# Kernel optimization log

Hardware: AMD Instinct MI355X
Metric: run time of the kernel (lower is better)

The kernel has to match this reference:

```python
import jax, jax.numpy as jnp
import numpy as np

TAU = 1.0  # initial_temperature, non-trainable
EPS = 1e-10


def setup_inputs() -> dict:
    key = jax.random.key(0)
    ks = jax.random.split(key, 5)
    B, D, E, A = 8192, 1024, 32, 128
    x = jax.random.normal(ks[0], (B, D), dtype=jnp.float32)
    W_att = jax.random.normal(ks[1], (E, D), dtype=jnp.float32) * (1.0 / np.sqrt(D))
    b_att = jnp.zeros((E,), dtype=jnp.float32)
    adaptive_bias = jnp.zeros((E,), dtype=jnp.float32)
    W_strat = jax.random.normal(ks[2], (E, A, D), dtype=jnp.float32) * (1.0 / np.sqrt(D))
    b_strat = jnp.zeros((E, A), dtype=jnp.float32)
    gumbel_u = jax.random.uniform(ks[3], (B, E), dtype=jnp.float32)
    return {"x": x, "W_att": W_att, "b_att": b_att, "adaptive_bias": adaptive_bias,
            "W_strat": W_strat, "b_strat": b_strat, "gumbel_u": gumbel_u}


def reference(x, W_att, b_att, adaptive_bias, W_strat, b_strat, gumbel_u):
    # Gating: linear + adaptive bias, then gumbel-softmax with temperature TAU
    logits = x @ W_att.T + b_att + adaptive_bias            # [B, E]
    g = -jnp.log(-jnp.log(gumbel_u + EPS) + EPS)            # gumbel noise [B, E]
    weights = jax.nn.softmax((logits + g) / TAU, axis=-1)   # [B, E] soft selection
    # Per-strategy outputs: each strategy is Linear(D -> A)
    strat_out = jnp.einsum('bd,ead->bea', x, W_strat) + b_strat  # [B, E, A]
    # Weighted combine (superposition)
    out = jnp.einsum('be,bea->ba', weights, strat_out)      # [B, A]
    return out
```

## Files before the change

### kernel.cpp

```cpp
#include <hip/hip_runtime.h>
#include <stdint.h>

typedef unsigned short u16;
typedef __attribute__((ext_vector_type(4))) float f32x4;
typedef __attribute__((ext_vector_type(8))) short short8;
typedef __attribute__((ext_vector_type(8))) unsigned short u16x8;

static constexpr int Bq = 8192;
static constexpr int Dq = 1024;
static constexpr int Eq = 32;
static constexpr int Aq = 128;
static constexpr int NSTRAT = 4096;

__device__ inline u16 f32_to_bf16_rne(float f) {
    uint32_t u = __float_as_uint(f);
    uint32_t r = 0x7fffu + ((u >> 16) & 1u);
    return (u16)((u + r) >> 16);
}
__device__ inline float bf16_to_f32(u16 h) {
    return __uint_as_float(((uint32_t)h) << 16);
}
__device__ inline void gload_lds16(const u16* g, u16* l) {
    __builtin_amdgcn_global_load_lds(
        (const __attribute__((address_space(1))) void*)g,
        (__attribute__((address_space(3))) void*)l, 16, 0, 0);
}

__global__ __launch_bounds__(256) void cvt_fused(const float* __restrict__ x,
                                                 const float* __restrict__ Ws,
                                                 u16* __restrict__ xb) {
    size_t i = ((size_t)blockIdx.x * 256 + threadIdx.x) * 8;
    const size_t XN = (size_t)Bq * Dq;
    const float* src;
    if (i < XN) {
        src = x + i;
    } else {
        size_t j = i - XN;
        int rp = (int)(j >> 10);
        int e = rp & 31;
        int a = rp >> 5;
        src = Ws + ((size_t)((e << 7) + a) << 10) + (j & 1023);
    }
    f32x4 a4 = *(const f32x4*)(src);
    f32x4 b4 = *(const f32x4*)(src + 4);
    u16x8 o;
    o[0] = f32_to_bf16_rne(a4[0]); o[1] = f32_to_bf16_rne(a4[1]);
    o[2] = f32_to_bf16_rne(a4[2]); o[3] = f32_to_bf16_rne(a4[3]);
    o[4] = f32_to_bf16_rne(b4[0]); o[5] = f32_to_bf16_rne(b4[1]);
    o[6] = f32_to_bf16_rne(b4[2]); o[7] = f32_to_bf16_rne(b4[3]);
    *(u16x8*)(xb + i) = o;
}

#define FBAR do { asm volatile("" ::: "memory"); __builtin_amdgcn_s_barrier(); asm volatile("" ::: "memory"); } while (0)
#define LGKM0 asm volatile("s_waitcnt lgkmcnt(0)" ::: "memory")
#define VMCNT(n) asm volatile("s_waitcnt vmcnt(" #n ")" ::: "memory")
#define SB __builtin_amdgcn_sched_barrier(0)
#define PRIO1 __builtin_amdgcn_s_setprio(1)
#define PRIO0 __builtin_amdgcn_s_setprio(0)
#define MF(a, b, c) __builtin_amdgcn_mfma_f32_16x16x32_bf16(a, b, c, 0, 0, 0)


#define STAGE_A(buf, h, kt) do { \
    gload_lds16(agA + (size_t)((h)*128) * 1024 + (size_t)(kt) * 64, (u16*)&lds[buf][h][tid * 8]); \
    gload_lds16(agA + (size_t)((h)*128 + 64) * 1024 + (size_t)(kt) * 64, (u16*)&lds[buf][h][4096 + tid * 8]); \
} while (0)
#define STAGE_B(buf, h, kt) do { \
    gload_lds16(agB + (size_t)((h)*128) * 1024 + (size_t)(kt) * 64, (u16*)&lds[buf][2 + (h)][tid * 8]); \
    gload_lds16(agB + (size_t)((h)*128 + 64) * 1024 + (size_t)(kt) * 64, (u16*)&lds[buf][2 + (h)][4096 + tid * 8]); \
} while (0)

#define LDA8(DST, ABASE, mq) do { \
    DST[0] = *(const short8*)((ABASE) + (mq)*4096 + 0*1024 + aoff0); \
    DST[1] = *(const short8*)((ABASE) + (mq)*4096 + 0*1024 + aoff1); \
    DST[2] = *(const short8*)((ABASE) + (mq)*4096 + 1*1024 + aoff0); \
    DST[3] = *(const short8*)((ABASE) + (mq)*4096 + 1*1024 + aoff1); \
    DST[4] = *(const short8*)((ABASE) + (mq)*4096 + 2*1024 + aoff0); \
    DST[5] = *(const short8*)((ABASE) + (mq)*4096 + 2*1024 + aoff1); \
    DST[6] = *(const short8*)((ABASE) + (mq)*4096 + 3*1024 + aoff0); \
    DST[7] = *(const short8*)((ABASE) + (mq)*4096 + 3*1024 + aoff1); \
} while (0)
#define LDB4(DST, BBASE, nq) do { \
    DST[0] = *(const short8*)((BBASE) + (nq)*2048 + 0*1024 + boff0); \
    DST[1] = *(const short8*)((BBASE) + (nq)*2048 + 0*1024 + boff1); \
    DST[2] = *(const short8*)((BBASE) + (nq)*2048 + 1*1024 + boff0); \
    DST[3] = *(const short8*)((BBASE) + (nq)*2048 + 1*1024 + boff1); \
} while (0)

#define QUAD(mq, nq, AS, BS) do { \
    acc[(mq)*4+0][(nq)*2+0] = MF(AS[0], BS[0], acc[(mq)*4+0][(nq)*2+0]); \
    acc[(mq)*4+0][(nq)*2+1] = MF(AS[0], BS[2], acc[(mq)*4+0][(nq)*2+1]); \
    acc[(mq)*4+1][(nq)*2+0] = MF(AS[2], BS[0], acc[(mq)*4+1][(nq)*2+0]); \
    acc[(mq)*4+1][(nq)*2+1] = MF(AS[2], BS[2], acc[(mq)*4+1][(nq)*2+1]); \
    acc[(mq)*4+2][(nq)*2+0] = MF(AS[4], BS[0], acc[(mq)*4+2][(nq)*2+0]); \
    acc[(mq)*4+2][(nq)*2+1] = MF(AS[4], BS[2], acc[(mq)*4+2][(nq)*2+1]); \
    acc[(mq)*4+3][(nq)*2+0] = MF(AS[6], BS[0], acc[(mq)*4+3][(nq)*2+0]); \
    acc[(mq)*4+3][(nq)*2+1] = MF(AS[6], BS[2], acc[(mq)*4+3][(nq)*2+1]); \
    acc[(mq)*4+0][(nq)*2+0] = MF(AS[1], BS[1], acc[(mq)*4+0][(nq)*2+0]); \
    acc[(mq)*4+0][(nq)*2+1] = MF(AS[1], BS[3], acc[(mq)*4+0][(nq)*2+1]); \
    acc[(mq)*4+1][(nq)*2+0] = MF(AS[3], BS[1], acc[(mq)*4+1][(nq)*2+0]); \
    acc[(mq)*4+1][(nq)*2+1] = MF(AS[3], BS[3], acc[(mq)*4+1][(nq)*2+1]); \
    acc[(mq)*4+2][(nq)*2+0] = MF(AS[5], BS[1], acc[(mq)*4+2][(nq)*2+0]); \
    acc[(mq)*4+2][(nq)*2+1] = MF(AS[5], BS[3], acc[(mq)*4+2][(nq)*2+1]); \
    acc[(mq)*4+3][(nq)*2+0] = MF(AS[7], BS[1], acc[(mq)*4+3][(nq)*2+0]); \
    acc[(mq)*4+3][(nq)*2+1] = MF(AS[7], BS[3], acc[(mq)*4+3][(nq)*2+1]); \
} while (0)

#define GITER(t, TAIL) do { \
     \
    LDB4(Bs0, Bbase0, 0); \
    STAGE_A(1, 0, (t) + 1); \
    SB; FBAR; LGKM0; SB; \
    PRIO1; QUAD(0, 0, As0, Bs0); PRIO0; SB; FBAR; \
     \
    LDB4(Bs1, Bbase0, 1); \
    STAGE_A(1, 1, (t) + 1); \
    SB; FBAR; LGKM0; SB; \
    PRIO1; QUAD(0, 1, As0, Bs1); PRIO0; SB; FBAR; \
     \
    LDA8(As1, Abase0, 1); \
    if (!(TAIL)) STAGE_B(0, 0, (t) + 2); \
    SB; FBAR; LGKM0; SB; \
    PRIO1; QUAD(1, 1, As1, Bs1); PRIO0; SB; \
    if (TAIL) { VMCNT(0); } else { VMCNT(2); } \
    FBAR; \
     \
    LDA8(As0, Abase1, 0); \
    if (!(TAIL)) STAGE_B(0, 1, (t) + 2); \
    SB; FBAR; LGKM0; SB; \
    PRIO1; QUAD(1, 0, As1, Bs0); PRIO0; SB; FBAR; \
     \
    LDB4(Bs0, Bbase1, 0); \
    if (!(TAIL)) STAGE_A(0, 0, (t) + 2); \
    SB; FBAR; LGKM0; SB; \
    PRIO1; QUAD(0, 0, As0, Bs0); PRIO0; SB; FBAR; \
     \
    LDB4(Bs1, Bbase1, 1); \
    if (!(TAIL)) STAGE_A(0, 1, (t) + 2); \
    SB; FBAR; LGKM0; SB; \
    PRIO1; QUAD(0, 1, As0, Bs1); PRIO0; SB; FBAR; \
     \
    LDA8(As1, Abase1, 1); \
    if (!(TAIL)) STAGE_B(1, 0, (t) + 3); \
    SB; FBAR; LGKM0; SB; \
    PRIO1; QUAD(1, 1, As1, Bs1); PRIO0; SB; \
    if (!(TAIL)) { VMCNT(2); } \
    FBAR; \
     \
    if (!(TAIL)) { LDA8(As0, Abase0, 0); STAGE_B(1, 1, (t) + 3); } \
    SB; FBAR; LGKM0; SB; \
    PRIO1; QUAD(1, 0, As1, Bs0); PRIO0; SB; FBAR; \
} while (0)

__global__ __launch_bounds__(512, 2) void gemm256(const u16* __restrict__ Abuf,
                                                  const u16* __restrict__ Bbuf,
                                                  const float* __restrict__ w,
                                                  const float* __restrict__ b_strat,
                                                  float* __restrict__ out) {
    __shared__ __align__(16) u16 lds[2][4][8192];

    const int tid = threadIdx.x;
    const int lane = tid & 63;
    const int wv = tid >> 6;
    const int wr = wv >> 2;
    const int wc = wv & 3;
    const int fr = lane & 15;
    const int fq = lane >> 4;

    const int bid = blockIdx.x;
    const int swz = (bid & 7) * 64 + (bid >> 3);
    const int m0 = (swz >> 4) * 256;
    const int n0 = (swz & 15) * 256;

    const int s_r = tid >> 3;
    const int s_c = ((tid & 7) * 8) ^ ((s_r & 7) << 3);
    const u16* agA = Abuf + (size_t)(m0 + s_r) * 1024 + s_c;
    const u16* agB = Bbuf + (size_t)(n0 + s_r) * 1024 + s_c;

    const int aoff0 = fr * 64 + ((fq ^ (fr & 7)) * 8);
    const int aoff1 = fr * 64 + (((fq + 4) ^ (fr & 7)) * 8);
    const int bof = (wc & 1) * 4096;
    const int boff0 = bof + aoff0;
    const int boff1 = bof + aoff1;

    const u16* Abase0 = (const u16*)&lds[0][wr][0];
    const u16* Abase1 = (const u16*)&lds[1][wr][0];
    const u16* Bbase0 = (const u16*)&lds[0][2 + (wc >> 1)][0];
    const u16* Bbase1 = (const u16*)&lds[1][2 + (wc >> 1)][0];

    f32x4 acc[8][4] = {};
    short8 As0[8], As1[8], Bs0[4], Bs1[4];

    STAGE_A(0, 0, 0); STAGE_A(0, 1, 0); STAGE_B(0, 0, 0); STAGE_B(0, 1, 0);
    STAGE_B(1, 0, 1); STAGE_B(1, 1, 1);
    SB; VMCNT(4); FBAR;
    LDA8(As0, Abase0, 0);

#pragma unroll 1
    for (int t = 0; t < 14; t += 2) { GITER(t, 0); }
    GITER(14, 1);

    const int crow = m0 + wr * 128 + fq * 4;
    const int a0 = (n0 >> 5) + wc * 2;
    const float bs00 = b_strat[fr * 128 + a0];
    const float bs10 = b_strat[(16 + fr) * 128 + a0];
    const float bs01 = b_strat[fr * 128 + a0 + 1];
    const float bs11 = b_strat[(16 + fr) * 128 + a0 + 1];
#pragma unroll
    for (int im = 0; im < 8; ++im) {
#pragma unroll
        for (int q = 0; q < 4; ++q) {
            const int row = crow + im * 16 + q;
            const float w0 = w[(size_t)row * 32 + fr];
            const float w1 = w[(size_t)row * 32 + 16 + fr];
            float v0 = w0 * (acc[im][0][q] + bs00) + w1 * (acc[im][1][q] + bs10);
            float v1 = w0 * (acc[im][2][q] + bs01) + w1 * (acc[im][3][q] + bs11);
#pragma unroll
            for (int s = 1; s < 16; s <<= 1) {
                v0 += __shfl_xor(v0, s);
                v1 += __shfl_xor(v1, s);
            }
            if (fr == 0) {
                out[(size_t)row * 128 + a0] = v0;
                out[(size_t)row * 128 + a0 + 1] = v1;
            }
        }
    }
}

__global__ __launch_bounds__(512) void logits_kernel(const u16* __restrict__ xb,
                                                     const float* __restrict__ W_att,
                                                     const float* __restrict__ b_att,
                                                     const float* __restrict__ abias,
                                                     const float* __restrict__ gu,
                                                     float* __restrict__ w) {
    __shared__ __align__(16) u16 Wa[32][1032];

    const int tid = threadIdx.x;
    const int lane = tid & 63;
    const int wv = tid >> 6;
    const int fr = lane & 15;
    const int fq = lane >> 4;
    const int m0 = blockIdx.x * 128;

    {
        const int row = tid >> 4;
        const int col0 = (tid & 15) * 64;
        const float* src = W_att + (size_t)row * 1024 + col0;
        u16* dst = &Wa[row][col0];
#pragma unroll
        for (int it = 0; it < 8; ++it) {
            f32x4 a = *(const f32x4*)(src + it * 8);
            f32x4 b = *(const f32x4*)(src + it * 8 + 4);
            u16x8 o;
            o[0] = f32_to_bf16_rne(a[0]); o[1] = f32_to_bf16_rne(a[1]);
            o[2] = f32_to_bf16_rne(a[2]); o[3] = f32_to_bf16_rne(a[3]);
            o[4] = f32_to_bf16_rne(b[0]); o[5] = f32_to_bf16_rne(b[1]);
            o[6] = f32_to_bf16_rne(b[2]); o[7] = f32_to_bf16_rne(b[3]);
            *(u16x8*)(dst + it * 8) = o;
        }
    }
    __syncthreads();

    f32x4 acc0 = {}, acc1 = {};
    const u16* xrow = xb + (size_t)(m0 + wv * 16 + fr) * 1024 + fq * 8;
#pragma unroll 4
    for (int k0 = 0; k0 < 1024; k0 += 32) {
        short8 a0 = *(const short8*)(xrow + k0);
        short8 b0 = *(const short8*)(&Wa[fr][k0 + fq * 8]);
        short8 b1 = *(const short8*)(&Wa[16 + fr][k0 + fq * 8]);
        acc0 = MF(a0, b0, acc0);
        acc1 = MF(a0, b1, acc1);
    }

    const float bba0 = b_att[fr] + abias[fr];
    const float bba1 = b_att[16 + fr] + abias[16 + fr];
#pragma unroll
    for (int q = 0; q < 4; ++q) {
        const int row = m0 + wv * 16 + fq * 4 + q;
        float u0 = gu[(size_t)row * 32 + fr];
        float u1 = gu[(size_t)row * 32 + 16 + fr];
        float g0 = -logf(-logf(u0 + 1e-10f) + 1e-10f);
        float g1 = -logf(-logf(u1 + 1e-10f) + 1e-10f);
        float z0 = acc0[q] + bba0 + g0;
        float z1 = acc1[q] + bba1 + g1;
        float mx = fmaxf(z0, z1);
#pragma unroll
        for (int s = 1; s < 16; s <<= 1) mx = fmaxf(mx, __shfl_xor(mx, s));
        float p0 = __expf(z0 - mx);
        float p1 = __expf(z1 - mx);
        float sm = p0 + p1;
#pragma unroll
        for (int s = 1; s < 16; s <<= 1) sm += __shfl_xor(sm, s);
        float inv = 1.0f / sm;
        w[(size_t)row * 32 + fr] = p0 * inv;
        w[(size_t)row * 32 + 16 + fr] = p1 * inv;
    }
}

extern "C" void kernel_launch(void* const* d_in, const int* in_sizes, int n_in,
                              void* d_out, int out_size, void* d_ws, size_t ws_size,
                              hipStream_t stream) {
    (void)in_sizes; (void)n_in; (void)out_size; (void)ws_size;
    const float* x       = (const float*)d_in[0];
    const float* W_att   = (const float*)d_in[1];
    const float* b_att   = (const float*)d_in[2];
    const float* abias   = (const float*)d_in[3];
    const float* W_strat = (const float*)d_in[4];
    const float* b_strat = (const float*)d_in[5];
    const float* gu      = (const float*)d_in[6];
    float* out = (float*)d_out;

    u16* xb = (u16*)d_ws;
    u16* Wb = xb + (size_t)Bq * Dq;
    float* w = (float*)(Wb + (size_t)NSTRAT * Dq);

    cvt_fused<<<(Bq * Dq + NSTRAT * Dq) / (256 * 8), 256, 0, stream>>>(x, W_strat, xb);

    logits_kernel<<<Bq / 128, 512, 0, stream>>>(xb, W_att, b_att, abias, gu, w);

    gemm256<<<512, 512, 0, stream>>>(xb, Wb, w, b_strat, out);
}
```

Baseline: 107.0 us.

## Merge bf16 conversion and gating logits into one launch; use DPP row reductions

```diff
diff --git a/kernel.cpp b/kernel.cpp
--- a/kernel.cpp
+++ b/kernel.cpp
@@ -25,30 +25,102 @@
         (const __attribute__((address_space(1))) void*)g,
         (__attribute__((address_space(3))) void*)l, 16, 0, 0);
 }
-
-__global__ __launch_bounds__(256) void cvt_fused(const float* __restrict__ x,
-                                                 const float* __restrict__ Ws,
-                                                 u16* __restrict__ xb) {
-    size_t i = ((size_t)blockIdx.x * 256 + threadIdx.x) * 8;
-    const size_t XN = (size_t)Bq * Dq;
-    const float* src;
-    if (i < XN) {
-        src = x + i;
+__device__ inline short8 cvt8(const float* p) {
+    f32x4 a = *(const f32x4*)p;
+    f32x4 b = *(const f32x4*)(p + 4);
+    short8 o;
+    o[0] = (short)f32_to_bf16_rne(a[0]); o[1] = (short)f32_to_bf16_rne(a[1]);
+    o[2] = (short)f32_to_bf16_rne(a[2]); o[3] = (short)f32_to_bf16_rne(a[3]);
+    o[4] = (short)f32_to_bf16_rne(b[0]); o[5] = (short)f32_to_bf16_rne(b[1]);
+    o[6] = (short)f32_to_bf16_rne(b[2]); o[7] = (short)f32_to_bf16_rne(b[3]);
+    return o;
+}
+template <int CTRL>
+__device__ inline float dppadd(float v) {
+    int t = __builtin_amdgcn_update_dpp(0, __float_as_int(v), CTRL, 0xf, 0xf, false);
+    return v + __int_as_float(t);
+}
+__device__ inline float red16(float v) {
+    v = dppadd<0xb1>(v);
+    v = dppadd<0x4e>(v);
+    v = dppadd<0x124>(v);
+    v = dppadd<0x128>(v);
+    return v;
+}
+
+#define MF(a, b, c) __builtin_amdgcn_mfma_f32_16x16x32_bf16(a, b, c, 0, 0, 0)
+
+__global__ __launch_bounds__(256) void cvt_logits(const float* __restrict__ x,
+                                                  const float* __restrict__ Ws,
+                                                  const float* __restrict__ W_att,
+                                                  const float* __restrict__ b_att,
+                                                  const float* __restrict__ abias,
+                                                  const float* __restrict__ gu,
+                                                  u16* __restrict__ xb,
+                                                  float* __restrict__ w) {
+    const int blk = blockIdx.x;
+    if (blk < 6144) {
+        size_t i = ((size_t)blk * 256 + threadIdx.x) * 8;
+        const size_t XN = (size_t)Bq * Dq;
+        const float* src;
+        if (i < XN) {
+            src = x + i;
+        } else {
+            size_t j = i - XN;
+            int rp = (int)(j >> 10);
+            int e = rp & 31;
+            int a = rp >> 5;
+            src = Ws + ((size_t)((e << 7) + a) << 10) + (j & 1023);
+        }
+        short8 o = cvt8(src);
+        *(short8*)(xb + i) = o;
     } else {
-        size_t j = i - XN;
-        int rp = (int)(j >> 10);
-        int e = rp & 31;
-        int a = rp >> 5;
-        src = Ws + ((size_t)((e << 7) + a) << 10) + (j & 1023);
+        const int tid = threadIdx.x;
+        const int lane = tid & 63;
+        const int wv = tid >> 6;
+        const int fr = lane & 15;
+        const int fq = lane >> 4;
+        const int m0 = (blk - 6144) * 64 + wv * 16;
+
+        const float* xrow = x + (size_t)(m0 + fr) * 1024;
+        const float* wa0 = W_att + (size_t)fr * 1024;
+        const float* wa1 = W_att + (size_t)(16 + fr) * 1024;
+
+        f32x4 acc0 = {}, acc1 = {};
+#pragma unroll 4
+        for (int k0 = 0; k0 < 1024; k0 += 32) {
+            const int kk = k0 + fq * 8;
+            short8 a0 = cvt8(xrow + kk);
+            short8 b0 = cvt8(wa0 + kk);
+            short8 b1 = cvt8(wa1 + kk);
+            acc0 = MF(a0, b0, acc0);
+            acc1 = MF(a0, b1, acc1);
+        }
+
+        const float bba0 = b_att[fr] + abias[fr];
+        const float bba1 = b_att[16 + fr] + abias[16 + fr];
+#pragma unroll
+        for (int q = 0; q < 4; ++q) {
+            const int row = m0 + fq * 4 + q;
+            float u0 = gu[(size_t)row * 32 + fr];
+            float u1 = gu[(size_t)row * 32 + 16 + fr];
+            float g0 = -logf(-logf(u0 + 1e-10f) + 1e-10f);
+            float g1 = -logf(-logf(u1 + 1e-10f) + 1e-10f);
+            float z0 = acc0[q] + bba0 + g0;
+            float z1 = acc1[q] + bba1 + g1;
+            float mx = fmaxf(z0, z1);
+#pragma unroll
+            for (int s = 1; s < 16; s <<= 1) mx = fmaxf(mx, __shfl_xor(mx, s));
+            float p0 = __expf(z0 - mx);
+            float p1 = __expf(z1 - mx);
+            float sm = p0 + p1;
+#pragma unroll
+            for (int s = 1; s < 16; s <<= 1) sm += __shfl_xor(sm, s);
+            float inv = 1.0f / sm;
+            w[(size_t)row * 32 + fr] = p0 * inv;
+            w[(size_t)row * 32 + 16 + fr] = p1 * inv;
+        }
     }
-    f32x4 a4 = *(const f32x4*)(src);
-    f32x4 b4 = *(const f32x4*)(src + 4);
-    u16x8 o;
-    o[0] = f32_to_bf16_rne(a4[0]); o[1] = f32_to_bf16_rne(a4[1]);
-    o[2] = f32_to_bf16_rne(a4[2]); o[3] = f32_to_bf16_rne(a4[3]);
-    o[4] = f32_to_bf16_rne(b4[0]); o[5] = f32_to_bf16_rne(b4[1]);
-    o[6] = f32_to_bf16_rne(b4[2]); o[7] = f32_to_bf16_rne(b4[3]);
-    *(u16x8*)(xb + i) = o;
 }
 
 #define FBAR do { asm volatile("" ::: "memory"); __builtin_amdgcn_s_barrier(); asm volatile("" ::: "memory"); } while (0)
@@ -57,7 +129,6 @@
 #define SB __builtin_amdgcn_sched_barrier(0)
 #define PRIO1 __builtin_amdgcn_s_setprio(1)
 #define PRIO0 __builtin_amdgcn_s_setprio(0)
-#define MF(a, b, c) __builtin_amdgcn_mfma_f32_16x16x32_bf16(a, b, c, 0, 0, 0)
 
 
 #define STAGE_A(buf, h, kt) do { \
@@ -214,86 +285,13 @@
             const float w1 = w[(size_t)row * 32 + 16 + fr];
             float v0 = w0 * (acc[im][0][q] + bs00) + w1 * (acc[im][1][q] + bs10);
             float v1 = w0 * (acc[im][2][q] + bs01) + w1 * (acc[im][3][q] + bs11);
-#pragma unroll
-            for (int s = 1; s < 16; s <<= 1) {
-                v0 += __shfl_xor(v0, s);
-                v1 += __shfl_xor(v1, s);
-            }
+            v0 = red16(v0);
+            v1 = red16(v1);
             if (fr == 0) {
                 out[(size_t)row * 128 + a0] = v0;
                 out[(size_t)row * 128 + a0 + 1] = v1;
             }
         }
-    }
-}
-
-__global__ __launch_bounds__(512) void logits_kernel(const u16* __restrict__ xb,
-                                                     const float* __restrict__ W_att,
-                                                     const float* __restrict__ b_att,
-                                                     const float* __restrict__ abias,
-                                                     const float* __restrict__ gu,
-                                                     float* __restrict__ w) {
-    __shared__ __align__(16) u16 Wa[32][1032];
-
-    const int tid = threadIdx.x;
-    const int lane = tid & 63;
-    const int wv = tid >> 6;
-    const int fr = lane & 15;
-    const int fq = lane >> 4;
-    const int m0 = blockIdx.x * 128;
-
-    {
-        const int row = tid >> 4;
-        const int col0 = (tid & 15) * 64;
-        const float* src = W_att + (size_t)row * 1024 + col0;
-        u16* dst = &Wa[row][col0];
-#pragma unroll
-        for (int it = 0; it < 8; ++it) {
-            f32x4 a = *(const f32x4*)(src + it * 8);
-            f32x4 b = *(const f32x4*)(src + it * 8 + 4);
-            u16x8 o;
-            o[0] = f32_to_bf16_rne(a[0]); o[1] = f32_to_bf16_rne(a[1]);
-            o[2] = f32_to_bf16_rne(a[2]); o[3] = f32_to_bf16_rne(a[3]);
-            o[4] = f32_to_bf16_rne(b[0]); o[5] = f32_to_bf16_rne(b[1]);
-            o[6] = f32_to_bf16_rne(b[2]); o[7] = f32_to_bf16_rne(b[3]);
-            *(u16x8*)(dst + it * 8) = o;
-        }
-    }
-    __syncthreads();
-
-    f32x4 acc0 = {}, acc1 = {};
-    const u16* xrow = xb + (size_t)(m0 + wv * 16 + fr) * 1024 + fq * 8;
-#pragma unroll 4
-    for (int k0 = 0; k0 < 1024; k0 += 32) {
-        short8 a0 = *(const short8*)(xrow + k0);
-        short8 b0 = *(const short8*)(&Wa[fr][k0 + fq * 8]);
-        short8 b1 = *(const short8*)(&Wa[16 + fr][k0 + fq * 8]);
-        acc0 = MF(a0, b0, acc0);
-        acc1 = MF(a0, b1, acc1);
-    }
-
-    const float bba0 = b_att[fr] + abias[fr];
-    const float bba1 = b_att[16 + fr] + abias[16 + fr];
-#pragma unroll
-    for (int q = 0; q < 4; ++q) {
-        const int row = m0 + wv * 16 + fq * 4 + q;
-        float u0 = gu[(size_t)row * 32 + fr];
-        float u1 = gu[(size_t)row * 32 + 16 + fr];
-        float g0 = -logf(-logf(u0 + 1e-10f) + 1e-10f);
-        float g1 = -logf(-logf(u1 + 1e-10f) + 1e-10f);
-        float z0 = acc0[q] + bba0 + g0;
-        float z1 = acc1[q] + bba1 + g1;
-        float mx = fmaxf(z0, z1);
-#pragma unroll
-        for (int s = 1; s < 16; s <<= 1) mx = fmaxf(mx, __shfl_xor(mx, s));
-        float p0 = __expf(z0 - mx);
-        float p1 = __expf(z1 - mx);
-        float sm = p0 + p1;
-#pragma unroll
-        for (int s = 1; s < 16; s <<= 1) sm += __shfl_xor(sm, s);
-        float inv = 1.0f / sm;
-        w[(size_t)row * 32 + fr] = p0 * inv;
-        w[(size_t)row * 32 + 16 + fr] = p1 * inv;
     }
 }
 
@@ -314,9 +312,7 @@
     u16* Wb = xb + (size_t)Bq * Dq;
     float* w = (float*)(Wb + (size_t)NSTRAT * Dq);
 
-    cvt_fused<<<(Bq * Dq + NSTRAT * Dq) / (256 * 8), 256, 0, stream>>>(x, W_strat, xb);
-
-    logits_kernel<<<Bq / 128, 512, 0, stream>>>(xb, W_att, b_att, abias, gu, w);
+    cvt_logits<<<6144 + 128, 256, 0, stream>>>(x, W_strat, W_att, b_att, abias, gu, xb, w);
 
     gemm256<<<512, 512, 0, stream>>>(xb, Wb, w, b_strat, out);
 }
```

New measurement: 149.6 us. +39.8%, slower.
